# Performance work log

Hardware: AMD Instinct MI355X
Metric: run time of the kernel (lower is better)

Reference implementation:

```python
import jax, jax.numpy as jnp
import numpy as np

HEAD_DIM = 64
NORM_EPS = 1e-5
W_SCALE = -0.6065306597126334  # -exp(-0.5)


def _rwkv7_scan(r, w, k, v, a, b):
    # r,w,k,a,b: [B,T,H,K]; v: [B,T,H,V]. Official RWKV7 recurrence (per head):
    #   S_t = S_{t-1} * diag(exp(w_t)) + (S_{t-1} @ a_t) b_t^T + v_t k_t^T ,  o_t = S_t @ r_t
    Bsz, T, H, K = r.shape
    V = v.shape[-1]
    decay = jnp.exp(w)

    def step(S, xs):
        r_t, d_t, k_t, v_t, a_t, b_t = xs
        sa = jnp.einsum('bhvk,bhk->bhv', S, a_t)
        S = S * d_t[:, :, None, :] + sa[..., None] * b_t[:, :, None, :] + v_t[..., None] * k_t[:, :, None, :]
        o_t = jnp.einsum('bhvk,bhk->bhv', S, r_t)
        return S, o_t

    xs = tuple(jnp.moveaxis(t, 1, 0) for t in (r, decay, k, v, a, b))
    S0 = jnp.zeros((Bsz, H, V, K), dtype=r.dtype)
    _, o = jax.lax.scan(step, S0, xs)
    return jnp.moveaxis(o, 0, 1)  # [B,T,H,V]


def setup_inputs() -> dict:
    key = jax.random.key(0)
    B, T, H = 2, 4096, 2048
    NH, DK, DV = 32, 64, 64
    D_DECAY, D_A, D_V, D_G = 96, 96, 64, 256
    ks = iter(jax.random.split(key, 40))
    n = lambda *s: jax.random.normal(next(ks), s, dtype=jnp.float32)
    u = lambda *s: jax.random.uniform(next(ks), s, dtype=jnp.float32)
    inp = {
        'hidden_states': n(B, T, H),
        'v_first': n(B, T, H),
        'x_r': u(1, 1, H), 'x_w': u(1, 1, H), 'x_k': u(1, 1, H),
        'x_v': u(1, 1, H), 'x_a': u(1, 1, H), 'x_g': u(1, 1, H),
        'k_k': 0.71 + 0.05 * n(H),
        'k_a': 1.02 + 0.05 * n(H),
        'r_k': -0.04 + 0.02 * n(NH, DK),
        'w_r': 0.02 * n(H, H), 'w_k': 0.002 * n(H, H),
        'w_v': 0.02 * n(H, H), 'w_o': 0.02 * n(H, H),
        'wA': 0.02 * n(D_DECAY, H), 'wB': 0.02 * n(H, D_DECAY), 'wb': -0.5 + 0.1 * n(H),
        'aA': 0.02 * n(D_A, H), 'aB': 0.02 * n(H, D_A), 'ab': 0.1 * n(H),
        'vA': 0.02 * n(D_V, H), 'vB': 0.02 * n(H, D_V), 'vb': 0.5 + 0.1 * n(H),
        'gA': 0.02 * n(D_G, H), 'gB': 0.02 * n(H, D_G),
        'gn_w': jnp.ones(H, jnp.float32),
        'gn_b': jnp.zeros(H, jnp.float32),
    }
    return inp


def reference(hidden_states, v_first, x_r, x_w, x_k, x_v, x_a, x_g,
              k_k, k_a, r_k, w_r, w_k, w_v, w_o,
              wA, wB, wb, aA, aB, ab, vA, vB, vb, gA, gB, gn_w, gn_b):
    B, T, H = hidden_states.shape
    NH, DK = r_k.shape
    DV = H // NH
    # token shift: delta = shift(x) - x (zero-padded at t=0)
    shifted = jnp.pad(hidden_states, ((0, 0), (1, 0), (0, 0)))[:, :-1]
    delta = shifted - hidden_states
    xr = hidden_states + delta * x_r
    xw = hidden_states + delta * x_w
    xk = hidden_states + delta * x_k
    xv = hidden_states + delta * x_v
    xa = hidden_states + delta * x_a
    xg = hidden_states + delta * x_g
    r = xr @ w_r.T
    w = W_SCALE * jax.nn.sigmoid(jnp.tanh(xw @ wA.T) @ wB.T + wb)  # log-decay in (-0.6065, 0)
    k = xk @ w_k.T
    v = xv @ w_v.T
    v = v + (v_first - v) * jax.nn.sigmoid((xv @ vA.T) @ vB.T + vb)  # lerp with v_first (layer_idx != 0)
    a = jax.nn.sigmoid((xa @ aA.T) @ aB.T + ab)
    g = jax.nn.sigmoid(xg @ gA.T) @ gB.T  # g_lora: sigmoid activation inside, no bias
    kk = (k * k_k).reshape(B, T, NH, DK)
    kk = kk / jnp.maximum(jnp.linalg.norm(kk, axis=-1, keepdims=True), 1e-12)
    k = k * (1.0 + (a - 1.0) * k_a)  # fused_k_rwkv7
    r4 = r.reshape(B, T, NH, DK)
    w4 = w.reshape(B, T, NH, DK)
    k4 = k.reshape(B, T, NH, DK)
    a4 = a.reshape(B, T, NH, DK)
    v4 = v.reshape(B, T, NH, DV)
    o = _rwkv7_scan(r4, w4, k4, v4, -kk, kk * a4)  # [B,T,NH,DV]
    # GroupNorm over each head (eps = head_dim * norm_eps)
    mu = o.mean(-1, keepdims=True)
    var = ((o - mu) ** 2).mean(-1, keepdims=True)
    on = (o - mu) / jnp.sqrt(var + HEAD_DIM * NORM_EPS)
    on = on * gn_w.reshape(NH, DV) + gn_b.reshape(NH, DV)
    on = on + (r4 * k4 * r_k).sum(-1, keepdims=True) * v4
    out = (on.reshape(B, T, H) * g) @ w_o.T
    return out
```

## Files before the change

kernel.cpp:

```cpp
#include <hip/hip_runtime.h>
#include <cstdint>
#include <cstddef>

typedef unsigned short u16;
typedef unsigned int u32;

typedef __bf16 bf8_t __attribute__((ext_vector_type(8)));
typedef float f4_t __attribute__((ext_vector_type(4)));

__device__ __forceinline__ u16 f2bf(float x) {
  u32 u = __float_as_uint(x);
  u = (u + 0x7fffu + ((u >> 16) & 1u)) >> 16;
  return (u16)u;
}
__device__ __forceinline__ float bf2f(u16 x) {
  u32 u = ((u32)x) << 16;
  return __uint_as_float(u);
}
__device__ __forceinline__ float sigf(float x) { return 1.f / (1.f + __expf(-x)); }

#define MFMA16(a, b, c) __builtin_amdgcn_mfma_f32_16x16x32_bf16(a, b, c, 0, 0, 0)

__global__ void fill_kernel(float* p, float v, long n) {
  long i = (long)blockIdx.x * blockDim.x + threadIdx.x;
  if (i < n) p[i] = v;
}

__global__ void padcvt_kernel(const float* __restrict__ src, u16* __restrict__ dst,
                              int rows, int cols, int pc, long total) {
  long i = (long)blockIdx.x * blockDim.x + threadIdx.x;
  if (i >= total) return;
  int r = (int)(i / pc), c = (int)(i % pc);
  float v = (r < rows && c < cols) ? src[(long)r * cols + c] : 0.f;
  dst[i] = f2bf(v);
}

__global__ void wf_kernel(const float* __restrict__ src, const float* __restrict__ coef,
                          u16* __restrict__ Wf, int rows_valid, int row0, long total) {
  long i = (long)blockIdx.x * blockDim.x + threadIdx.x;
  if (i >= total) return;
  int r = (int)(i >> 12);
  int k = (int)(i & 4095);
  float v = 0.f;
  if (r < rows_valid) {
    int kk = k & 2047;
    v = src[(long)r * 2048 + kk];
    if (k >= 2048) v *= coef[kk];
  }
  Wf[(long)(row0 + r) * 4096 + k] = f2bf(v);
}

__global__ void hd_kernel(const float* __restrict__ h_b, u16* __restrict__ out_seg,
                          int t0, int Tc, long total4) {
  long i = (long)blockIdx.x * blockDim.x + threadIdx.x;
  if (i >= total4) return;
  long e = i * 4;
  const int H = 2048;
  int col = (int)(e % H);
  int tl = (int)(e / H);
  int tg = t0 + tl;
  const float* hp = h_b + (long)tg * H + col;
  float4 hv = *(const float4*)hp;
  float4 pv = make_float4(0.f, 0.f, 0.f, 0.f);
  if (tg > 0) pv = *(const float4*)(hp - H);
  u16* row = out_seg + (long)tl * 4096;
  uint2 ph, pd;
  ph.x = (u32)f2bf(hv.x) | ((u32)f2bf(hv.y) << 16);
  ph.y = (u32)f2bf(hv.z) | ((u32)f2bf(hv.w) << 16);
  pd.x = (u32)f2bf(pv.x - hv.x) | ((u32)f2bf(pv.y - hv.y) << 16);
  pd.y = (u32)f2bf(pv.z - hv.z) | ((u32)f2bf(pv.w - hv.w) << 16);
  *(uint2*)(row + col) = ph;
  *(uint2*)(row + 2048 + col) = pd;
}

__global__ void mix1_kernel(const float* __restrict__ h_b, const float* __restrict__ coef,
                            u16* __restrict__ out_seg, int t0, int Tc, long total4) {
  long i = (long)blockIdx.x * blockDim.x + threadIdx.x;
  if (i >= total4) return;
  long e = i * 4;
  const int H = 2048;
  int col = (int)(e % H);
  int tl = (int)(e / H);
  int tg = t0 + tl;
  const float* hp = h_b + (long)tg * H + col;
  float4 hv = *(const float4*)hp;
  float4 pv = make_float4(0.f, 0.f, 0.f, 0.f);
  if (tg > 0) pv = *(const float4*)(hp - H);
  float4 cc = *(const float4*)(coef + col);
  uint2 pk;
  pk.x = (u32)f2bf(hv.x + (pv.x - hv.x) * cc.x) | ((u32)f2bf(hv.y + (pv.y - hv.y) * cc.y) << 16);
  pk.y = (u32)f2bf(hv.z + (pv.z - hv.z) * cc.z) | ((u32)f2bf(hv.w + (pv.w - hv.w) * cc.w) << 16);
  *(uint2*)(out_seg + e) = pk;
}

#define LDSW 40
template <int MODE>
__global__ __launch_bounds__(256) void gemm_bt(
    const u16* __restrict__ A, const u16* __restrict__ B, void* __restrict__ Cv,
    int M, int N, int K, int lda, const float* __restrict__ aux1) {
  __shared__ u16 sA[128 * LDSW];
  __shared__ u16 sB[128 * LDSW];
  const int tid = threadIdx.x;
  const long bm = (long)blockIdx.y * 128;
  const long bn = (long)blockIdx.x * 128;
  const int wave = tid >> 6, lane = tid & 63;
  const int wm = (wave >> 1) * 64, wn = (wave & 1) * 64;
  const int quad = lane >> 4, rr = lane & 15;

  f4_t acc[4][4];
  const f4_t zero = {0.f, 0.f, 0.f, 0.f};
#pragma unroll
  for (int i = 0; i < 4; i++)
#pragma unroll
    for (int j = 0; j < 4; j++) acc[i][j] = zero;

  const int c0 = tid, c1 = tid + 256;
  const u16* pa0 = A + (bm + (c0 >> 2)) * (long)lda + (c0 & 3) * 8;
  const u16* pa1 = A + (bm + (c1 >> 2)) * (long)lda + (c1 & 3) * 8;
  const u16* pb0 = B + (bn + (c0 >> 2)) * (long)K + (c0 & 3) * 8;
  const u16* pb1 = B + (bn + (c1 >> 2)) * (long)K + (c1 & 3) * 8;

  uint4 ra0, ra1, rb0, rb1;
#define LDG(k0)                              \
  {                                          \
    ra0 = *(const uint4*)(pa0 + (k0));       \
    ra1 = *(const uint4*)(pa1 + (k0));       \
    rb0 = *(const uint4*)(pb0 + (k0));       \
    rb1 = *(const uint4*)(pb1 + (k0));       \
  }
  LDG(0);
  for (int k0 = 0; k0 < K; k0 += 32) {
    __syncthreads();
    *(uint4*)(&sA[(c0 >> 2) * LDSW + (c0 & 3) * 8]) = ra0;
    *(uint4*)(&sA[(c1 >> 2) * LDSW + (c1 & 3) * 8]) = ra1;
    *(uint4*)(&sB[(c0 >> 2) * LDSW + (c0 & 3) * 8]) = rb0;
    *(uint4*)(&sB[(c1 >> 2) * LDSW + (c1 & 3) * 8]) = rb1;
    __syncthreads();
    if (k0 + 32 < K) LDG(k0 + 32);
    bf8_t af[4], bfv[4];
#pragma unroll
    for (int i = 0; i < 4; i++)
      af[i] = *(const bf8_t*)(&sA[(wm + i * 16 + rr) * LDSW + quad * 8]);
#pragma unroll
    for (int j = 0; j < 4; j++)
      bfv[j] = *(const bf8_t*)(&sB[(wn + j * 16 + rr) * LDSW + quad * 8]);
#pragma unroll
    for (int i = 0; i < 4; i++)
#pragma unroll
      for (int j = 0; j < 4; j++)
        acc[i][j] = MFMA16(af[i], bfv[j], acc[i][j]);
  }
#undef LDG
#pragma unroll
  for (int i = 0; i < 4; i++)
#pragma unroll
    for (int j = 0; j < 4; j++)
#pragma unroll
      for (int rg = 0; rg < 4; rg++) {
        long m = bm + wm + i * 16 + quad * 4 + rg;
        long n = bn + wn + j * 16 + rr;
        long id = m * (long)N + n;
        float x = acc[i][j][rg];
        if (MODE == 0) ((float*)Cv)[id] = x;
        else if (MODE == 1) ((u16*)Cv)[id] = f2bf(x);
        else if (MODE == 2) ((u16*)Cv)[id] = f2bf(tanhf(x));
        else if (MODE == 3) ((u16*)Cv)[id] = f2bf(sigf(x));
        else if (MODE == 5) {
          float y = (n < 128) ? tanhf(x) : ((n < 384) ? x : sigf(x));
          ((u16*)Cv)[id] = f2bf(y);
        } else if (MODE == 6) {
          ((u16*)Cv)[id] = f2bf(sigf(x + aux1[(int)n]));
        }
      }
}

__device__ __forceinline__ void gload16(const u16* g, u16* l) {
  __builtin_amdgcn_global_load_lds((const __attribute__((address_space(1))) u32*)g,
                                   (__attribute__((address_space(3))) u32*)l, 16, 0, 0);
}

template <int MODE>
__global__ __launch_bounds__(512, 2) void gemm256_bt(
    const u16* __restrict__ A, const u16* __restrict__ Bw, void* __restrict__ Cv,
    int M, int N, int K, int rsp, long r0off, long r1off) {
  __shared__ u16 L[2][2][2][8192];
  const int tid = threadIdx.x;
  const int lane = tid & 63, w = tid >> 6;
  const int quad = lane >> 4, l15 = lane & 15;
  const long bm = (long)blockIdx.y * 256, bn = (long)blockIdx.x * 256;
  const int wm = (w >> 2) * 128, wn = (w & 3) * 64;
  const int NT = K >> 6;

  const int u0 = tid, u1 = tid + 512;
  const int ar0 = u0 >> 2, ar1 = u1 >> 2;
  const int aq0 = (u0 & 3) ^ (ar0 & 3), aq1 = (u1 & 3) ^ (ar1 & 3);
  const u16* gA0 = A + (bm + ar0) * (long)K + aq0 * 8;
  const u16* gA1 = A + (bm + ar1) * (long)K + aq1 * 8;
  const u16* gB0 = Bw + (bn + ar0) * (long)K + aq0 * 8;
  const u16* gB1 = Bw + (bn + ar1) * (long)K + aq1 * 8;

  const int qx = (quad ^ (l15 & 3)) * 8;
  const int roA = (wm + l15) * 32 + qx;
  const int roB = (wn + l15) * 32 + qx;

  f4_t acc[8][4];
#pragma unroll
  for (int i = 0; i < 8; i++)
#pragma unroll
    for (int j = 0; j < 4; j++) acc[i][j] = (f4_t){0.f, 0.f, 0.f, 0.f};

#define STG_A(buf, s, tt)                                   \
  {                                                         \
    long ko = ((long)(tt) << 6) + ((s) << 5);               \
    gload16(gA0 + ko, &L[buf][0][s][u0 * 8]);               \
    gload16(gA1 + ko, &L[buf][0][s][u1 * 8]);               \
  }
#define STG_B(buf, s, tt)                                   \
  {                                                         \
    long ko = ((long)(tt) << 6) + ((s) << 5);               \
    gload16(gB0 + ko, &L[buf][1][s][u0 * 8]);               \
    gload16(gB1 + ko, &L[buf][1][s][u1 * 8]);               \
  }
#define LDA4(P, o)                                          \
  _Pragma("unroll") for (int i = 0; i < 4; i++)             \
      aF[i] = *(const bf8_t*)((P) + roA + ((o) + i) * 512);
#define LDB4(P)                                             \
  _Pragma("unroll") for (int j = 0; j < 4; j++)             \
      bF[j] = *(const bf8_t*)((P) + roB + j * 512);
#define MFMA_BLK(base)                                      \
  __builtin_amdgcn_s_setprio(1);                            \
  _Pragma("unroll") for (int i = 0; i < 4; i++)             \
      _Pragma("unroll") for (int j = 0; j < 4; j++)         \
          acc[(base) + i][j] = MFMA16(aF[i], bF[j], acc[(base) + i][j]); \
  __builtin_amdgcn_s_setprio(0);
#define SBAR __builtin_amdgcn_s_barrier()

  STG_A(0, 0, 0); STG_B(0, 0, 0);
  STG_A(0, 1, 0); STG_B(0, 1, 0);
  if (NT > 1) { STG_A(1, 0, 1); STG_B(1, 0, 1); }
  asm volatile("s_waitcnt vmcnt(8)" ::: "memory");
  SBAR;

  bf8_t aF[4], bF[4];
  for (int t = 0; t < NT; ++t) {
    const int buf = t & 1;
    const u16* A0 = &L[buf][0][0][0];
    const u16* B0 = &L[buf][1][0][0];
    const u16* A1 = &L[buf][0][1][0];
    const u16* B1 = &L[buf][1][1][0];
    LDA4(A0, 0);
    LDB4(B0);
    if (t + 1 < NT) STG_A(buf ^ 1, 1, t + 1);
    SBAR;
    asm volatile("s_waitcnt lgkmcnt(0)" ::: "memory");
    MFMA_BLK(0);
    SBAR;
    LDA4(A0, 4);
    if (t + 1 < NT) STG_B(buf ^ 1, 1, t + 1);
    SBAR;
    asm volatile("s_waitcnt lgkmcnt(0)" ::: "memory");
    MFMA_BLK(4);
    if (t == NT - 1) asm volatile("s_waitcnt vmcnt(0)" ::: "memory");
    else asm volatile("s_waitcnt vmcnt(8)" ::: "memory");
    SBAR;
    LDA4(A1, 0);
    LDB4(B1);
    if (t + 2 < NT) STG_A(buf, 0, t + 2);
    SBAR;
    asm volatile("s_waitcnt lgkmcnt(0)" ::: "memory");
    MFMA_BLK(0);
    SBAR;
    LDA4(A1, 4);
    if (t + 2 < NT) STG_B(buf, 0, t + 2);
    SBAR;
    asm volatile("s_waitcnt lgkmcnt(0)" ::: "memory");
    MFMA_BLK(4);
    if (t == NT - 2) asm volatile("s_waitcnt vmcnt(4)" ::: "memory");
    else if (t < NT - 2) asm volatile("s_waitcnt vmcnt(8)" ::: "memory");
    SBAR;
  }

#pragma unroll
  for (int i = 0; i < 8; i++) {
#pragma unroll
    for (int rg = 0; rg < 4; rg++) {
      long mm = bm + wm + i * 16 + quad * 4 + rg;
      long crow = (mm < rsp) ? (mm + r0off) : (mm + r1off);
#pragma unroll
      for (int j = 0; j < 4; j++) {
        long n = bn + wn + j * 16 + l15;
        float x = acc[i][j][rg];
        if (MODE == 0) ((float*)Cv)[crow * (long)N + n] = x;
        else ((u16*)Cv)[crow * (long)N + n] = f2bf(x);
      }
    }
  }
#undef STG_A
#undef STG_B
#undef LDA4
#undef LDB4
#undef MFMA_BLK
#undef SBAR
}

__global__ __launch_bounds__(256) void post1_kernel(
    const float* __restrict__ F1, const float* __restrict__ F4, float* F0,
    const float* __restrict__ F2, const u16* __restrict__ VL,
    const float* __restrict__ vfirst,
    u16* __restrict__ KM, u16* __restrict__ KK, u16* __restrict__ BB, u16* __restrict__ VB,
    const float* __restrict__ k_k, const float* __restrict__ k_a,
    const float* __restrict__ wb, const float* __restrict__ ab, int t0, int Tc) {
  const int lane = threadIdx.x & 63;
  const long th = (((long)blockIdx.x * 256) + threadIdx.x) >> 6;
  const int hcol = (int)(th & 31) * 64 + lane;
  const long idx = th * 64 + lane;
  const long r = th >> 5;
  float kraw = F1[idx];
  float kk0 = kraw * k_k[hcol];
  float ss = kk0 * kk0;
#pragma unroll
  for (int m = 32; m; m >>= 1) ss += __shfl_xor(ss, m, 64);
  float kkn = kk0 / fmaxf(sqrtf(ss), 1e-12f);
  float av = sigf(F4[idx] + ab[hcol]);
  float w = -0.6065306597126334f * sigf(F0[idx] + wb[hcol]);
  F0[idx] = w;
  KM[idx] = f2bf(kraw * (1.f + (av - 1.f) * k_a[hcol]));
  KK[idx] = f2bf(kkn);
  BB[idx] = f2bf(kkn * av);
  float vraw = F2[idx];
  float sg = bf2f(VL[idx]);
  long vfi = ((r / Tc) * 4096 + t0 + (r % Tc)) * 2048 + hcol;
  VB[idx] = f2bf(vraw + (vfirst[vfi] - vraw) * sg);
}

constexpr int ST64 = 72;
constexpr int ST32 = 40;
constexpr int STX = 132;

__global__ __launch_bounds__(64) void phaseA_kernel(
    const float* __restrict__ wS, const u16* __restrict__ kmS, const u16* __restrict__ kkS,
    const u16* __restrict__ bbS, const u16* __restrict__ vbS, const u16* __restrict__ rbS,
    float* __restrict__ POWb, u16* __restrict__ PAb, float* __restrict__ Zb,
    u16* __restrict__ GTb, float* __restrict__ CLb, int Tc, int sp0) {
  __shared__ u16 lXa[16 * ST64], lXr[16 * ST64], lYa[16 * ST64], lYb[16 * ST64];
  __shared__ u16 lYaT[64 * ST32], lYbT[64 * ST32], lVmT[64 * ST32];
  __shared__ u16 lTWt[64 * ST32], lTAt[64 * ST32];
  __shared__ u16 lP[16 * ST32], lQ[16 * ST32], lBm[16 * ST32];
  __shared__ float lA[16 * 16];
  __shared__ float lX[16 * STX];
  __shared__ float lcl[64];
  const int lane = threadIdx.x;
  const int quad = lane >> 4, l15 = lane & 15;
  const long tile = blockIdx.x;
  const int bh = (int)(tile & 63);
  const int col = (int)(tile >> 6);
  const int b = bh >> 5, h = bh & 31;
  const long s = tile;
  const f4_t z4 = {0.f, 0.f, 0.f, 0.f};

  {
    u32* p0 = (u32*)&lYaT[lane * ST32 + 16];
    u32* p1 = (u32*)&lYbT[lane * ST32 + 16];
    u32* p2 = (u32*)&lVmT[lane * ST32 + 16];
    u32* p3 = (u32*)&lTWt[lane * ST32 + 16];
    u32* p4 = (u32*)&lTAt[lane * ST32 + 16];
#pragma unroll
    for (int q = 0; q < 8; q++) { p0[q] = 0; p1[q] = 0; p2[q] = 0; p3[q] = 0; p4[q] = 0; }
    if (lane < 16) {
      u32* q0 = (u32*)&lP[lane * ST32 + 16];
      u32* q1 = (u32*)&lQ[lane * ST32 + 16];
      u32* q2 = (u32*)&lBm[lane * ST32 + 16];
#pragma unroll
      for (int q = 0; q < 8; q++) { q0[q] = 0; q1[q] = 0; q2[q] = 0; }
    }
  }

  const long rowbase = (long)b * Tc + (long)(sp0 + col) * 16;
  const long gbase = rowbase * 2048 + (long)h * 64 + lane;
  float cw = 0.f;
#pragma unroll
  for (int i = 0; i < 16; i++) {
    long g = gbase + (long)i * 2048;
    float w = wS[g];
    float km = bf2f(kmS[g]), kk = bf2f(kkS[g]), bb = bf2f(bbS[g]);
    float vv = bf2f(vbS[g]), rr2 = bf2f(rbS[g]);
    float cwm = cw;
    cw += w;
    float E1 = __expf(cwm), E2 = __expf(-cw), E3 = __expf(cw);
    float xa = -kk * E1;
    lXa[i * ST64 + lane] = f2bf(xa);
    lX[i * STX + 64 + lane] = xa;
    lXr[i * ST64 + lane] = f2bf(rr2 * E3);
    float ya = bb * E2, yb = km * E2;
    lYa[i * ST64 + lane] = f2bf(ya);
    lYb[i * ST64 + lane] = f2bf(yb);
    lYaT[lane * ST32 + i] = f2bf(ya);
    lYbT[lane * ST32 + i] = f2bf(yb);
    lVmT[lane * ST32 + i] = f2bf(vv);
    if (i == 15) { lcl[lane] = E3; CLb[s * 64 + lane] = E3; }
  }
  __syncthreads();

  {
    f4_t aA = z4, aB = z4, aP = z4, aQ = z4;
#pragma unroll
    for (int kc = 0; kc < 2; kc++) {
      bf8_t xa = *(const bf8_t*)&lXa[l15 * ST64 + quad * 8 + 32 * kc];
      bf8_t xr = *(const bf8_t*)&lXr[l15 * ST64 + quad * 8 + 32 * kc];
      bf8_t ya = *(const bf8_t*)&lYa[l15 * ST64 + quad * 8 + 32 * kc];
      bf8_t yb = *(const bf8_t*)&lYb[l15 * ST64 + quad * 8 + 32 * kc];
      aA = MFMA16(xa, ya, aA);
      aB = MFMA16(xa, yb, aB);
      aP = MFMA16(xr, ya, aP);
      aQ = MFMA16(xr, yb, aQ);
    }
#pragma unroll
    for (int rg = 0; rg < 4; rg++) {
      int m = quad * 4 + rg;
      lA[m * 16 + l15] = (l15 < m) ? aA[rg] : 0.f;
      lBm[m * ST32 + l15] = (l15 < m) ? f2bf(aB[rg]) : (u16)0;
      lP[m * ST32 + l15] = (l15 <= m) ? f2bf(aP[rg]) : (u16)0;
      lQ[m * ST32 + l15] = (l15 <= m) ? f2bf(aQ[rg]) : (u16)0;
    }
  }
  __syncthreads();

#pragma unroll
  for (int nt = 0; nt < 4; nt++) {
    f4_t acc = z4;
    bf8_t a = *(const bf8_t*)&lBm[l15 * ST32 + quad * 8];
    bf8_t bb2 = *(const bf8_t*)&lVmT[(nt * 16 + l15) * ST32 + quad * 8];
    acc = MFMA16(a, bb2, acc);
#pragma unroll
    for (int rg = 0; rg < 4; rg++) lX[(quad * 4 + rg) * STX + nt * 16 + l15] = acc[rg];
  }
  __syncthreads();

  for (int i = 1; i < 16; i++) {
    float x0 = lX[i * STX + lane], x1 = lX[i * STX + 64 + lane];
    for (int j = 0; j < i; j++) {
      float aij = lA[i * 16 + j];
      x0 += aij * lX[j * STX + lane];
      x1 += aij * lX[j * STX + 64 + lane];
    }
    lX[i * STX + lane] = x0;
    lX[i * STX + 64 + lane] = x1;
  }
#pragma unroll
  for (int i = 0; i < 16; i++) {
    lTWt[lane * ST32 + i] = f2bf(lX[i * STX + lane]);
    lTAt[lane * ST32 + i] = f2bf(lX[i * STX + 64 + lane]);
  }
  __syncthreads();

#pragma unroll
  for (int nt = 0; nt < 4; nt++) {
    f4_t acc = z4;
    bf8_t p = *(const bf8_t*)&lP[l15 * ST32 + quad * 8];
    bf8_t q = *(const bf8_t*)&lQ[l15 * ST32 + quad * 8];
    bf8_t tw = *(const bf8_t*)&lTWt[(nt * 16 + l15) * ST32 + quad * 8];
    bf8_t vm = *(const bf8_t*)&lVmT[(nt * 16 + l15) * ST32 + quad * 8];
    acc = MFMA16(p, tw, acc);
    acc = MFMA16(q, vm, acc);
#pragma unroll
    for (int rg = 0; rg < 4; rg++)
      POWb[s * 1024 + (quad * 4 + rg) * 64 + nt * 16 + l15] = acc[rg];
  }
#pragma unroll
  for (int nt = 0; nt < 4; nt++) {
    f4_t acc = z4;
    bf8_t p = *(const bf8_t*)&lP[l15 * ST32 + quad * 8];
    bf8_t ta = *(const bf8_t*)&lTAt[(nt * 16 + l15) * ST32 + quad * 8];
    acc = MFMA16(p, ta, acc);
#pragma unroll
    for (int rg = 0; rg < 4; rg++) {
      float xr = bf2f(lXr[(quad * 4 + rg) * ST64 + nt * 16 + l15]);
      PAb[s * 1024 + (quad * 4 + rg) * 64 + nt * 16 + l15] = f2bf(acc[rg] + xr);
    }
  }

#pragma unroll
  for (int mt = 0; mt < 4; mt++)
#pragma unroll
    for (int nt = 0; nt < 4; nt++) {
      f4_t acc = z4;
      bf8_t tw = *(const bf8_t*)&lTWt[(mt * 16 + l15) * ST32 + quad * 8];
      bf8_t vm = *(const bf8_t*)&lVmT[(mt * 16 + l15) * ST32 + quad * 8];
      bf8_t yat = *(const bf8_t*)&lYaT[(nt * 16 + l15) * ST32 + quad * 8];
      bf8_t ybt = *(const bf8_t*)&lYbT[(nt * 16 + l15) * ST32 + quad * 8];
      acc = MFMA16(tw, yat, acc);
      acc = MFMA16(vm, ybt, acc);
      float cl = lcl[nt * 16 + l15];
#pragma unroll
      for (int rg = 0; rg < 4; rg++)
        Zb[s * 4096 + (mt * 16 + quad * 4 + rg) * 64 + nt * 16 + l15] = acc[rg] * cl;
    }
#pragma unroll
  for (int mt = 0; mt < 4; mt++)
#pragma unroll
    for (int nt = 0; nt < 4; nt++) {
      f4_t acc = z4;
      bf8_t yat = *(const bf8_t*)&lYaT[(mt * 16 + l15) * ST32 + quad * 8];
      bf8_t ta = *(const bf8_t*)&lTAt[(nt * 16 + l15) * ST32 + quad * 8];
      acc = MFMA16(yat, ta, acc);
#pragma unroll
      for (int rg = 0; rg < 4; rg++) {
        float cl = lcl[mt * 16 + quad * 4 + rg];
        GTb[s * 4096 + (mt * 16 + quad * 4 + rg) * 64 + nt * 16 + l15] = f2bf(acc[rg] * cl);
      }
    }
}

__global__ __launch_bounds__(256) void phaseB_kernel(
    const float* __restrict__ Zb, const u16* __restrict__ GTb, const float* __restrict__ CLb,
    u16* __restrict__ S0b, float* __restrict__ state, int CT, int init) {
  __shared__ u16 Sb[64 * ST64];
  const int bh = blockIdx.x;
  const int tid = threadIdx.x, wv = tid >> 6, lane = tid & 63;
  const int quad = lane >> 4, l15 = lane & 15;
  float S[4][4];
  if (init) {
#pragma unroll
    for (int nt = 0; nt < 4; nt++)
#pragma unroll
      for (int rg = 0; rg < 4; rg++) S[nt][rg] = 0.f;
  } else {
#pragma unroll
    for (int nt = 0; nt < 4; nt++)
#pragma unroll
      for (int rg = 0; rg < 4; rg++)
        S[nt][rg] = state[(long)bh * 4096 + (16 * wv + quad * 4 + rg) * 64 + nt * 16 + l15];
  }
  const f4_t z4 = {0.f, 0.f, 0.f, 0.f};
  for (int c = 0; c < CT; c++) {
    long s = (long)c * 64 + bh;
#pragma unroll
    for (int nt = 0; nt < 4; nt++)
#pragma unroll
      for (int rg = 0; rg < 4; rg++)
        Sb[(16 * wv + quad * 4 + rg) * ST64 + nt * 16 + l15] = f2bf(S[nt][rg]);
    __syncthreads();
    f4_t acc[4] = {z4, z4, z4, z4};
#pragma unroll
    for (int kc = 0; kc < 2; kc++) {
      bf8_t a = *(const bf8_t*)&Sb[(16 * wv + l15) * ST64 + quad * 8 + 32 * kc];
      *(uint4*)(S0b + s * 4096 + (16 * wv + l15) * 64 + quad * 8 + 32 * kc) = *(uint4*)&a;
#pragma unroll
      for (int nt = 0; nt < 4; nt++) {
        bf8_t g = *(const bf8_t*)(GTb + s * 4096 + (nt * 16 + l15) * 64 + quad * 8 + 32 * kc);
        acc[nt] = MFMA16(a, g, acc[nt]);
      }
    }
#pragma unroll
    for (int nt = 0; nt < 4; nt++) {
      float cl = CLb[s * 64 + nt * 16 + l15];
#pragma unroll
      for (int rg = 0; rg < 4; rg++) {
        float z = Zb[s * 4096 + (16 * wv + quad * 4 + rg) * 64 + nt * 16 + l15];
        S[nt][rg] = S[nt][rg] * cl + acc[nt][rg] + z;
      }
    }
    __syncthreads();
  }
#pragma unroll
  for (int nt = 0; nt < 4; nt++)
#pragma unroll
    for (int rg = 0; rg < 4; rg++)
      state[(long)bh * 4096 + (16 * wv + quad * 4 + rg) * 64 + nt * 16 + l15] = S[nt][rg];
}

__global__ __launch_bounds__(64) void phaseC_kernel(
    const float* __restrict__ POWb, const u16* __restrict__ PAb, const u16* __restrict__ S0b,
    float* __restrict__ O, int Tc, int sp0) {
  const int lane = threadIdx.x, quad = lane >> 4, l15 = lane & 15;
  const long tile = blockIdx.x;
  const int bh = (int)(tile & 63), col = (int)(tile >> 6);
  const int b = bh >> 5, h = bh & 31;
  const long s = tile;
  const f4_t z4 = {0.f, 0.f, 0.f, 0.f};
  f4_t acc[4] = {z4, z4, z4, z4};
#pragma unroll
  for (int kc = 0; kc < 2; kc++) {
    bf8_t a = *(const bf8_t*)(PAb + s * 1024 + l15 * 64 + quad * 8 + 32 * kc);
#pragma unroll
    for (int nt = 0; nt < 4; nt++) {
      bf8_t bo = *(const bf8_t*)(S0b + s * 4096 + (nt * 16 + l15) * 64 + quad * 8 + 32 * kc);
      acc[nt] = MFMA16(a, bo, acc[nt]);
    }
  }
  const long rowbase = (long)b * Tc + (long)(sp0 + col) * 16;
#pragma unroll
  for (int nt = 0; nt < 4; nt++)
#pragma unroll
    for (int rg = 0; rg < 4; rg++) {
      int i = quad * 4 + rg, v = nt * 16 + l15;
      float p = POWb[s * 1024 + i * 64 + v];
      O[(rowbase + i) * 2048 + (long)h * 64 + v] = p + acc[nt][rg];
    }
}

__global__ __launch_bounds__(256) void epi_kernel(
    const float* __restrict__ o, const u16* __restrict__ r, const u16* __restrict__ k,
    const u16* __restrict__ v, const u16* __restrict__ g,
    const float* __restrict__ r_k, const float* __restrict__ gn_w, const float* __restrict__ gn_b,
    u16* __restrict__ y) {
  const int lane = threadIdx.x & 63;
  const long th = (((long)blockIdx.x * 256) + threadIdx.x) >> 6;
  const int hcol = (int)(th & 31) * 64 + lane;
  const long idx = th * 64 + lane;
  float ov = o[idx];
  float s = ov;
#pragma unroll
  for (int m = 32; m; m >>= 1) s += __shfl_xor(s, m, 64);
  float mu = s * (1.f / 64.f);
  float d = ov - mu;
  float vs = d * d;
#pragma unroll
  for (int m = 32; m; m >>= 1) vs += __shfl_xor(vs, m, 64);
  float on = d * rsqrtf(vs * (1.f / 64.f) + 6.4e-4f);
  on = on * gn_w[hcol] + gn_b[hcol];
  float rk = bf2f(r[idx]) * bf2f(k[idx]) * r_k[hcol];
#pragma unroll
  for (int m = 32; m; m >>= 1) rk += __shfl_xor(rk, m, 64);
  on += rk * bf2f(v[idx]);
  y[idx] = f2bf(on * bf2f(g[idx]));
}

extern "C" void kernel_launch(void* const* d_in, const int* in_sizes, int n_in,
                              void* d_out, int out_size, void* d_ws, size_t ws_size,
                              hipStream_t stream) {
  constexpr int B = 2, T = 4096, H = 2048;
  const float* hst    = (const float*)d_in[0];
  const float* vfirst = (const float*)d_in[1];
  const float* x_r = (const float*)d_in[2];
  const float* x_w = (const float*)d_in[3];
  const float* x_k = (const float*)d_in[4];
  const float* x_v = (const float*)d_in[5];
  const float* x_a = (const float*)d_in[6];
  const float* x_g = (const float*)d_in[7];
  const float* k_k = (const float*)d_in[8];
  const float* k_a = (const float*)d_in[9];
  const float* r_k = (const float*)d_in[10];
  const float* w_r = (const float*)d_in[11];
  const float* w_k = (const float*)d_in[12];
  const float* w_v = (const float*)d_in[13];
  const float* w_o = (const float*)d_in[14];
  const float* wA  = (const float*)d_in[15];
  const float* wB  = (const float*)d_in[16];
  const float* wb  = (const float*)d_in[17];
  const float* aA  = (const float*)d_in[18];
  const float* aB  = (const float*)d_in[19];
  const float* ab  = (const float*)d_in[20];
  const float* vA  = (const float*)d_in[21];
  const float* vB  = (const float*)d_in[22];
  const float* vb  = (const float*)d_in[23];
  const float* gA  = (const float*)d_in[24];
  const float* gB  = (const float*)d_in[25];
  const float* gn_w= (const float*)d_in[26];
  const float* gn_b= (const float*)d_in[27];

  const size_t WEIGHT_BYTES = 4 * (size_t)H * H * 2 + 3 * (size_t)H * 128 * 2
                            + (size_t)H * 256 * 2 + (size_t)768 * 4096 * 2;
  const size_t STATE_BYTES = (size_t)64 * 4096 * 4;
  const size_t TILE_BYTES = 4096 + 2048 + 16384 + 8192 + 256 + 8192;

  int NC = -1, CT = 0;
  for (int pass = 0; pass < 2 && NC < 0; pass++) {
    for (int nc : {1, 2, 4, 8, 16}) {
      long Tc_ = T / nc;
      long R_ = (long)B * Tc_;
      long RH_ = R_ * H;
      size_t base = (size_t)RH_ * 16 + (size_t)RH_ * 16 + (size_t)RH_ * 4 + (size_t)R_ * 1536
                  + WEIGHT_BYTES + STATE_BYTES + (4 << 20);
      int cols = (int)(Tc_ / 16);
      int found = 0;
      for (int ct : {64, 32, 16, 8}) {
        if (ct > cols) continue;
        if (pass == 0 && ct < 16) continue;
        size_t need = base + (size_t)64 * ct * TILE_BYTES;
        if (need <= ws_size) { NC = nc; CT = ct; found = 1; break; }
      }
      if (found) break;
    }
  }
  const int BS = 256;
  auto cdiv = [](long a, long b) { return (int)((a + b - 1) / b); };
  if (NC < 0) {
    fill_kernel<<<cdiv(out_size, BS), BS, 0, stream>>>(
        (float*)d_out, 200000.f + (float)(ws_size >> 20), out_size);
    return;
  }
  const int Tc = T / NC;
  const long R = (long)B * Tc;
  const long RH = R * H;
  const int cols = Tc / 16;
  const int NTILE = 64 * CT;

  char* ws = (char*)d_ws;
  size_t off = 0;
  auto alloc = [&](size_t bytes) -> void* {
    void* p = ws + off;
    off += (bytes + 255) & ~(size_t)255;
    return p;
  };
  float* F0 = (float*)alloc(RH * 4);
  float* F1 = (float*)alloc(RH * 4);
  float* F2 = (float*)alloc(RH * 4);
  float* F4 = (float*)alloc(RH * 4);
  u16* KM  = (u16*)alloc(RH * 2);
  u16* KK  = (u16*)alloc(RH * 2);
  u16* BBs = (u16*)alloc(RH * 2);
  u16* VBs = (u16*)alloc(RH * 2);
  u16* RBs = (u16*)alloc(RH * 2);
  u16* MIXB = (u16*)alloc(RH * 2);
  u16* G    = (u16*)alloc(RH * 2);
  u16* VL   = (u16*)alloc(RH * 2);
  u16* HD   = (u16*)alloc(RH * 4);
  u16* s1all = (u16*)alloc(R * 1536);
  u16* wrb = (u16*)alloc((size_t)H * H * 2);
  u16* wkb = (u16*)alloc((size_t)H * H * 2);
  u16* wvb = (u16*)alloc((size_t)H * H * 2);
  u16* wob = (u16*)alloc((size_t)H * H * 2);
  u16* wBb = (u16*)alloc((size_t)H * 128 * 2);
  u16* aBb = (u16*)alloc((size_t)H * 128 * 2);
  u16* vBb = (u16*)alloc((size_t)H * 128 * 2);
  u16* gBb = (u16*)alloc((size_t)H * 256 * 2);
  u16* Wf  = (u16*)alloc((size_t)768 * 4096 * 2);
  float* state = (float*)alloc(STATE_BYTES);
  float* POWb = (float*)alloc((size_t)NTILE * 4096);
  u16*   PAb  = (u16*)alloc((size_t)NTILE * 2048);
  float* Zb   = (float*)alloc((size_t)NTILE * 16384);
  u16*   GTb  = (u16*)alloc((size_t)NTILE * 8192);
  float* CLb  = (float*)alloc((size_t)NTILE * 256);
  u16*   S0b  = (u16*)alloc((size_t)NTILE * 8192);
  float* Ob = F1;

  padcvt_kernel<<<cdiv((long)H * H, BS), BS, 0, stream>>>(w_r, wrb, H, H, H, (long)H * H);
  padcvt_kernel<<<cdiv((long)H * H, BS), BS, 0, stream>>>(w_k, wkb, H, H, H, (long)H * H);
  padcvt_kernel<<<cdiv((long)H * H, BS), BS, 0, stream>>>(w_v, wvb, H, H, H, (long)H * H);
  padcvt_kernel<<<cdiv((long)H * H, BS), BS, 0, stream>>>(w_o, wob, H, H, H, (long)H * H);
  padcvt_kernel<<<cdiv((long)H * 128, BS), BS, 0, stream>>>(wB, wBb, H, 96, 128, (long)H * 128);
  padcvt_kernel<<<cdiv((long)H * 128, BS), BS, 0, stream>>>(aB, aBb, H, 96, 128, (long)H * 128);
  padcvt_kernel<<<cdiv((long)H * 128, BS), BS, 0, stream>>>(vB, vBb, H, 64, 128, (long)H * 128);
  padcvt_kernel<<<cdiv((long)H * 256, BS), BS, 0, stream>>>(gB, gBb, H, 256, 256, (long)H * 256);
  wf_kernel<<<cdiv((long)128 * 4096, BS), BS, 0, stream>>>(wA, x_w, Wf, 96, 0, (long)128 * 4096);
  wf_kernel<<<cdiv((long)128 * 4096, BS), BS, 0, stream>>>(aA, x_a, Wf, 96, 128, (long)128 * 4096);
  wf_kernel<<<cdiv((long)128 * 4096, BS), BS, 0, stream>>>(vA, x_v, Wf, 64, 256, (long)128 * 4096);
  wf_kernel<<<cdiv((long)384 * 4096, BS), BS, 0, stream>>>(gA, x_g, Wf, 256, 384, (long)384 * 4096);

  const long mixTot = (long)Tc * H / 4;
  const int mixG = cdiv(mixTot, BS);
  const int ehG = (int)(R * 32 / 4);

  for (int c = 0; c < NC; c++) {
    const int t0 = c * Tc;
    auto MIX = [&](const float* coef) {
      for (int b = 0; b < B; b++)
        mix1_kernel<<<mixG, BS, 0, stream>>>(hst + (long)b * T * H, coef,
                                             MIXB + (long)b * Tc * H, t0, Tc, mixTot);
    };
    dim3 gBig(16, (unsigned)(R / 128)), gF(6, (unsigned)(R / 128));
    dim3 g256((unsigned)(H / 256), (unsigned)(R / 256));

    for (int b = 0; b < B; b++)
      hd_kernel<<<mixG, BS, 0, stream>>>(hst + (long)b * T * H,
                                         HD + (long)b * Tc * 4096, t0, Tc, mixTot);
    gemm_bt<5><<<gF, 256, 0, stream>>>(HD, Wf, s1all, (int)R, 768, 4096, 4096, nullptr);
    gemm_bt<0><<<gBig, 256, 0, stream>>>(s1all, wBb, F0, (int)R, H, 128, 768, nullptr);
    gemm_bt<0><<<gBig, 256, 0, stream>>>(s1all + 128, aBb, F4, (int)R, H, 128, 768, nullptr);
    MIX(x_v);
    gemm256_bt<0><<<g256, 512, 0, stream>>>(MIXB, wvb, F2, (int)R, H, H, (int)R, 0, 0);
    gemm_bt<6><<<gBig, 256, 0, stream>>>(s1all + 256, vBb, VL, (int)R, H, 128, 768, vb);
    gemm_bt<1><<<gBig, 256, 0, stream>>>(s1all + 384, gBb, G, (int)R, H, 256, 768, nullptr);
    MIX(x_r);
    gemm256_bt<1><<<g256, 512, 0, stream>>>(MIXB, wrb, RBs, (int)R, H, H, (int)R, 0, 0);
    MIX(x_k);
    gemm256_bt<0><<<g256, 512, 0, stream>>>(MIXB, wkb, F1, (int)R, H, H, (int)R, 0, 0);
    post1_kernel<<<ehG, 256, 0, stream>>>(F1, F4, F0, F2, VL, vfirst,
                                          KM, KK, BBs, VBs, k_k, k_a, wb, ab, t0, Tc);
    for (int sp = 0; sp < cols; sp += CT) {
      phaseA_kernel<<<NTILE, 64, 0, stream>>>(F0, KM, KK, BBs, VBs, RBs,
                                              POWb, PAb, Zb, GTb, CLb, Tc, sp);
      phaseB_kernel<<<64, 256, 0, stream>>>(Zb, GTb, CLb, S0b, state, CT,
                                            (c == 0 && sp == 0) ? 1 : 0);
      phaseC_kernel<<<NTILE, 64, 0, stream>>>(POWb, PAb, S0b, Ob, Tc, sp);
    }
    epi_kernel<<<ehG, 256, 0, stream>>>(Ob, RBs, KM, VBs, G, r_k, gn_w, gn_b, MIXB);
    gemm256_bt<0><<<g256, 512, 0, stream>>>(MIXB, wob, (float*)d_out, (int)R, H, H,
                                            Tc, (long)t0, (long)T - Tc + t0);
  }
}
```

Before: 2.852 ms.

## Prefetch phaseB chunk inputs, double-buffer gemm_bt loads, merge decay/a LoRA GEMMs

```diff
diff --git a/kernel.cpp b/kernel.cpp
--- a/kernel.cpp
+++ b/kernel.cpp
@@ -48,6 +48,17 @@
     if (k >= 2048) v *= coef[kk];
   }
   Wf[(long)(row0 + r) * 4096 + k] = f2bf(v);
+}
+
+__global__ void wab_kernel(const float* __restrict__ wB, const float* __restrict__ aB,
+                           u16* __restrict__ Wab, long total) {
+  long i = (long)blockIdx.x * blockDim.x + threadIdx.x;
+  if (i >= total) return;
+  int r = (int)(i >> 8), k = (int)(i & 255);
+  float v = 0.f;
+  if (r < 2048) { if (k < 96) v = wB[(long)r * 96 + k]; }
+  else { int rr = r - 2048; if (k >= 128 && k < 224) v = aB[(long)rr * 96 + (k - 128)]; }
+  Wab[i] = f2bf(v);
 }
 
 __global__ void hd_kernel(const float* __restrict__ h_b, u16* __restrict__ out_seg,
@@ -120,37 +131,58 @@
   const u16* pb0 = B + (bn + (c0 >> 2)) * (long)K + (c0 & 3) * 8;
   const u16* pb1 = B + (bn + (c1 >> 2)) * (long)K + (c1 & 3) * 8;
 
-  uint4 ra0, ra1, rb0, rb1;
-#define LDG(k0)                              \
-  {                                          \
-    ra0 = *(const uint4*)(pa0 + (k0));       \
-    ra1 = *(const uint4*)(pa1 + (k0));       \
-    rb0 = *(const uint4*)(pb0 + (k0));       \
-    rb1 = *(const uint4*)(pb1 + (k0));       \
-  }
-  LDG(0);
-  for (int k0 = 0; k0 < K; k0 += 32) {
+  uint4 a0A, a1A, b0A, b1A, a0B, a1B, b0B, b1B;
+#define LDGA(k0)                            \
+  {                                         \
+    a0A = *(const uint4*)(pa0 + (k0));      \
+    a1A = *(const uint4*)(pa1 + (k0));      \
+    b0A = *(const uint4*)(pb0 + (k0));      \
+    b1A = *(const uint4*)(pb1 + (k0));      \
+  }
+#define LDGB(k0)                            \
+  {                                         \
+    a0B = *(const uint4*)(pa0 + (k0));      \
+    a1B = *(const uint4*)(pa1 + (k0));      \
+    b0B = *(const uint4*)(pb0 + (k0));      \
+    b1B = *(const uint4*)(pb1 + (k0));      \
+  }
+#define STLDS(ra0, ra1, rb0, rb1)                          \
+  {                                                        \
+    *(uint4*)(&sA[(c0 >> 2) * LDSW + (c0 & 3) * 8]) = ra0; \
+    *(uint4*)(&sA[(c1 >> 2) * LDSW + (c1 & 3) * 8]) = ra1; \
+    *(uint4*)(&sB[(c0 >> 2) * LDSW + (c0 & 3) * 8]) = rb0; \
+    *(uint4*)(&sB[(c1 >> 2) * LDSW + (c1 & 3) * 8]) = rb1; \
+  }
+#define COMPUTE                                                        \
+  {                                                                    \
+    bf8_t af[4], bfv[4];                                               \
+    _Pragma("unroll") for (int i = 0; i < 4; i++)                      \
+        af[i] = *(const bf8_t*)(&sA[(wm + i * 16 + rr) * LDSW + quad * 8]); \
+    _Pragma("unroll") for (int j = 0; j < 4; j++)                      \
+        bfv[j] = *(const bf8_t*)(&sB[(wn + j * 16 + rr) * LDSW + quad * 8]); \
+    _Pragma("unroll") for (int i = 0; i < 4; i++)                      \
+        _Pragma("unroll") for (int j = 0; j < 4; j++)                  \
+            acc[i][j] = MFMA16(af[i], bfv[j], acc[i][j]);              \
+  }
+
+  LDGA(0);
+  LDGB(32);
+  for (int k0 = 0; k0 < K; k0 += 64) {
     __syncthreads();
-    *(uint4*)(&sA[(c0 >> 2) * LDSW + (c0 & 3) * 8]) = ra0;
-    *(uint4*)(&sA[(c1 >> 2) * LDSW + (c1 & 3) * 8]) = ra1;
-    *(uint4*)(&sB[(c0 >> 2) * LDSW + (c0 & 3) * 8]) = rb0;
-    *(uint4*)(&sB[(c1 >> 2) * LDSW + (c1 & 3) * 8]) = rb1;
+    STLDS(a0A, a1A, b0A, b1A);
     __syncthreads();
-    if (k0 + 32 < K) LDG(k0 + 32);
-    bf8_t af[4], bfv[4];
-#pragma unroll
-    for (int i = 0; i < 4; i++)
-      af[i] = *(const bf8_t*)(&sA[(wm + i * 16 + rr) * LDSW + quad * 8]);
-#pragma unroll
-    for (int j = 0; j < 4; j++)
-      bfv[j] = *(const bf8_t*)(&sB[(wn + j * 16 + rr) * LDSW + quad * 8]);
-#pragma unroll
-    for (int i = 0; i < 4; i++)
-#pragma unroll
-      for (int j = 0; j < 4; j++)
-        acc[i][j] = MFMA16(af[i], bfv[j], acc[i][j]);
-  }
-#undef LDG
+    if (k0 + 64 < K) LDGA(k0 + 64);
+    COMPUTE;
+    __syncthreads();
+    STLDS(a0B, a1B, b0B, b1B);
+    __syncthreads();
+    if (k0 + 96 < K) LDGB(k0 + 96);
+    COMPUTE;
+  }
+#undef LDGA
+#undef LDGB
+#undef STLDS
+#undef COMPUTE
 #pragma unroll
   for (int i = 0; i < 4; i++)
 #pragma unroll
@@ -304,7 +336,7 @@
 }
 
 __global__ __launch_bounds__(256) void post1_kernel(
-    const float* __restrict__ F1, const float* __restrict__ F4, float* F0,
+    const float* __restrict__ F1, const float* __restrict__ F0F4, float* __restrict__ W,
     const float* __restrict__ F2, const u16* __restrict__ VL,
     const float* __restrict__ vfirst,
     u16* __restrict__ KM, u16* __restrict__ KK, u16* __restrict__ BB, u16* __restrict__ VB,
@@ -321,9 +353,11 @@
 #pragma unroll
   for (int m = 32; m; m >>= 1) ss += __shfl_xor(ss, m, 64);
   float kkn = kk0 / fmaxf(sqrtf(ss), 1e-12f);
-  float av = sigf(F4[idx] + ab[hcol]);
-  float w = -0.6065306597126334f * sigf(F0[idx] + wb[hcol]);
-  F0[idx] = w;
+  float wlog = F0F4[r * 4096 + hcol];
+  float alog = F0F4[r * 4096 + 2048 + hcol];
+  float av = sigf(alog + ab[hcol]);
+  float w = -0.6065306597126334f * sigf(wlog + wb[hcol]);
+  W[idx] = w;
   KM[idx] = f2bf(kraw * (1.f + (av - 1.f) * k_a[hcol]));
   KK[idx] = f2bf(kkn);
   BB[idx] = f2bf(kkn * av);
@@ -532,36 +566,52 @@
         S[nt][rg] = state[(long)bh * 4096 + (16 * wv + quad * 4 + rg) * 64 + nt * 16 + l15];
   }
   const f4_t z4 = {0.f, 0.f, 0.f, 0.f};
-  for (int c = 0; c < CT; c++) {
-    long s = (long)c * 64 + bh;
-#pragma unroll
-    for (int nt = 0; nt < 4; nt++)
-#pragma unroll
-      for (int rg = 0; rg < 4; rg++)
-        Sb[(16 * wv + quad * 4 + rg) * ST64 + nt * 16 + l15] = f2bf(S[nt][rg]);
-    __syncthreads();
-    f4_t acc[4] = {z4, z4, z4, z4};
-#pragma unroll
-    for (int kc = 0; kc < 2; kc++) {
-      bf8_t a = *(const bf8_t*)&Sb[(16 * wv + l15) * ST64 + quad * 8 + 32 * kc];
-      *(uint4*)(S0b + s * 4096 + (16 * wv + l15) * 64 + quad * 8 + 32 * kc) = *(uint4*)&a;
-#pragma unroll
-      for (int nt = 0; nt < 4; nt++) {
-        bf8_t g = *(const bf8_t*)(GTb + s * 4096 + (nt * 16 + l15) * 64 + quad * 8 + 32 * kc);
-        acc[nt] = MFMA16(a, g, acc[nt]);
-      }
-    }
-#pragma unroll
-    for (int nt = 0; nt < 4; nt++) {
-      float cl = CLb[s * 64 + nt * 16 + l15];
-#pragma unroll
-      for (int rg = 0; rg < 4; rg++) {
-        float z = Zb[s * 4096 + (16 * wv + quad * 4 + rg) * 64 + nt * 16 + l15];
-        S[nt][rg] = S[nt][rg] * cl + acc[nt][rg] + z;
-      }
-    }
-    __syncthreads();
-  }
+
+  uint4 gtA[2][4], gtB[2][4];
+  float zA[4][4], zB[4][4], clA[4], clB[4];
+
+#define LOADSET(cc, gt, z, cl)                                                      \
+  {                                                                                 \
+    long s2 = (long)(cc) * 64 + bh;                                                 \
+    _Pragma("unroll") for (int kc = 0; kc < 2; kc++)                                \
+        _Pragma("unroll") for (int nt = 0; nt < 4; nt++)                            \
+            gt[kc][nt] = *(const uint4*)(GTb + s2 * 4096 + (nt * 16 + l15) * 64 + quad * 8 + 32 * kc); \
+    _Pragma("unroll") for (int nt = 0; nt < 4; nt++) {                              \
+      cl[nt] = CLb[s2 * 64 + nt * 16 + l15];                                        \
+      _Pragma("unroll") for (int rg = 0; rg < 4; rg++)                              \
+          z[nt][rg] = Zb[s2 * 4096 + (16 * wv + quad * 4 + rg) * 64 + nt * 16 + l15]; \
+    }                                                                               \
+  }
+#define BSTEP(cc, gt, z, cl, gtN, zN, clN, pf)                                      \
+  {                                                                                 \
+    long s1 = (long)(cc) * 64 + bh;                                                 \
+    _Pragma("unroll") for (int nt = 0; nt < 4; nt++)                                \
+        _Pragma("unroll") for (int rg = 0; rg < 4; rg++)                            \
+            Sb[(16 * wv + quad * 4 + rg) * ST64 + nt * 16 + l15] = f2bf(S[nt][rg]); \
+    __syncthreads();                                                                \
+    if (pf) LOADSET((cc) + 1, gtN, zN, clN);                                        \
+    f4_t acc[4] = {z4, z4, z4, z4};                                                 \
+    _Pragma("unroll") for (int kc = 0; kc < 2; kc++) {                              \
+      bf8_t a = *(const bf8_t*)&Sb[(16 * wv + l15) * ST64 + quad * 8 + 32 * kc];    \
+      *(uint4*)(S0b + s1 * 4096 + (16 * wv + l15) * 64 + quad * 8 + 32 * kc) = *(uint4*)&a; \
+      _Pragma("unroll") for (int nt = 0; nt < 4; nt++) {                            \
+        bf8_t g = *(const bf8_t*)&gt[kc][nt];                                       \
+        acc[nt] = MFMA16(a, g, acc[nt]);                                            \
+      }                                                                             \
+    }                                                                               \
+    _Pragma("unroll") for (int nt = 0; nt < 4; nt++)                                \
+        _Pragma("unroll") for (int rg = 0; rg < 4; rg++)                            \
+            S[nt][rg] = S[nt][rg] * cl[nt] + acc[nt][rg] + z[nt][rg];               \
+    __syncthreads();                                                                \
+  }
+
+  LOADSET(0, gtA, zA, clA);
+  for (int c = 0; c < CT; c += 2) {
+    BSTEP(c, gtA, zA, clA, gtB, zB, clB, (c + 1 < CT));
+    BSTEP(c + 1, gtB, zB, clB, gtA, zA, clA, (c + 2 < CT));
+  }
+#undef LOADSET
+#undef BSTEP
 #pragma unroll
   for (int nt = 0; nt < 4; nt++)
 #pragma unroll
@@ -659,8 +709,9 @@
   const float* gn_w= (const float*)d_in[26];
   const float* gn_b= (const float*)d_in[27];
 
-  const size_t WEIGHT_BYTES = 4 * (size_t)H * H * 2 + 3 * (size_t)H * 128 * 2
-                            + (size_t)H * 256 * 2 + (size_t)768 * 4096 * 2;
+  const size_t WEIGHT_BYTES = 4 * (size_t)H * H * 2 + (size_t)H * 128 * 2
+                            + (size_t)H * 256 * 2 + (size_t)768 * 4096 * 2
+                            + (size_t)4096 * 256 * 2;
   const size_t STATE_BYTES = (size_t)64 * 4096 * 4;
   const size_t TILE_BYTES = 4096 + 2048 + 16384 + 8192 + 256 + 8192;
 
@@ -670,7 +721,7 @@
       long Tc_ = T / nc;
       long R_ = (long)B * Tc_;
       long RH_ = R_ * H;
-      size_t base = (size_t)RH_ * 16 + (size_t)RH_ * 16 + (size_t)RH_ * 4 + (size_t)R_ * 1536
+      size_t base = (size_t)RH_ * 40 + (size_t)R_ * 1536
                   + WEIGHT_BYTES + STATE_BYTES + (4 << 20);
       int cols = (int)(Tc_ / 16);
       int found = 0;
@@ -703,10 +754,10 @@
     off += (bytes + 255) & ~(size_t)255;
     return p;
   };
-  float* F0 = (float*)alloc(RH * 4);
+  float* F0F4 = (float*)alloc(RH * 8);
   float* F1 = (float*)alloc(RH * 4);
   float* F2 = (float*)alloc(RH * 4);
-  float* F4 = (float*)alloc(RH * 4);
+  float* W  = (float*)alloc(RH * 4);
   u16* KM  = (u16*)alloc(RH * 2);
   u16* KK  = (u16*)alloc(RH * 2);
   u16* BBs = (u16*)alloc(RH * 2);
@@ -721,11 +772,10 @@
   u16* wkb = (u16*)alloc((size_t)H * H * 2);
   u16* wvb = (u16*)alloc((size_t)H * H * 2);
   u16* wob = (u16*)alloc((size_t)H * H * 2);
-  u16* wBb = (u16*)alloc((size_t)H * 128 * 2);
-  u16* aBb = (u16*)alloc((size_t)H * 128 * 2);
   u16* vBb = (u16*)alloc((size_t)H * 128 * 2);
   u16* gBb = (u16*)alloc((size_t)H * 256 * 2);
   u16* Wf  = (u16*)alloc((size_t)768 * 4096 * 2);
+  u16* Wab = (u16*)alloc((size_t)4096 * 256 * 2);
   float* state = (float*)alloc(STATE_BYTES);
   float* POWb = (float*)alloc((size_t)NTILE * 4096);
   u16*   PAb  = (u16*)alloc((size_t)NTILE * 2048);
@@ -739,14 +789,13 @@
   padcvt_kernel<<<cdiv((long)H * H, BS), BS, 0, stream>>>(w_k, wkb, H, H, H, (long)H * H);
   padcvt_kernel<<<cdiv((long)H * H, BS), BS, 0, stream>>>(w_v, wvb, H, H, H, (long)H * H);
   padcvt_kernel<<<cdiv((long)H * H, BS), BS, 0, stream>>>(w_o, wob, H, H, H, (long)H * H);
-  padcvt_kernel<<<cdiv((long)H * 128, BS), BS, 0, stream>>>(wB, wBb, H, 96, 128, (long)H * 128);
-  padcvt_kernel<<<cdiv((long)H * 128, BS), BS, 0, stream>>>(aB, aBb, H, 96, 128, (long)H * 128);
   padcvt_kernel<<<cdiv((long)H * 128, BS), BS, 0, stream>>>(vB, vBb, H, 64, 128, (long)H * 128);
   padcvt_kernel<<<cdiv((long)H * 256, BS), BS, 0, stream>>>(gB, gBb, H, 256, 256, (long)H * 256);
   wf_kernel<<<cdiv((long)128 * 4096, BS), BS, 0, stream>>>(wA, x_w, Wf, 96, 0, (long)128 * 4096);
   wf_kernel<<<cdiv((long)128 * 4096, BS), BS, 0, stream>>>(aA, x_a, Wf, 96, 128, (long)128 * 4096);
   wf_kernel<<<cdiv((long)128 * 4096, BS), BS, 0, stream>>>(vA, x_v, Wf, 64, 256, (long)128 * 4096);
   wf_kernel<<<cdiv((long)384 * 4096, BS), BS, 0, stream>>>(gA, x_g, Wf, 256, 384, (long)384 * 4096);
+  wab_kernel<<<cdiv((long)4096 * 256, BS), BS, 0, stream>>>(wB, aB, Wab, (long)4096 * 256);
 
   const long mixTot = (long)Tc * H / 4;
   const int mixG = cdiv(mixTot, BS);
@@ -759,15 +808,14 @@
         mix1_kernel<<<mixG, BS, 0, stream>>>(hst + (long)b * T * H, coef,
                                              MIXB + (long)b * Tc * H, t0, Tc, mixTot);
     };
-    dim3 gBig(16, (unsigned)(R / 128)), gF(6, (unsigned)(R / 128));
+    dim3 gBig(16, (unsigned)(R / 128)), gF(6, (unsigned)(R / 128)), gWA(32, (unsigned)(R / 128));
     dim3 g256((unsigned)(H / 256), (unsigned)(R / 256));
 
     for (int b = 0; b < B; b++)
       hd_kernel<<<mixG, BS, 0, stream>>>(hst + (long)b * T * H,
                                          HD + (long)b * Tc * 4096, t0, Tc, mixTot);
     gemm_bt<5><<<gF, 256, 0, stream>>>(HD, Wf, s1all, (int)R, 768, 4096, 4096, nullptr);
-    gemm_bt<0><<<gBig, 256, 0, stream>>>(s1all, wBb, F0, (int)R, H, 128, 768, nullptr);
-    gemm_bt<0><<<gBig, 256, 0, stream>>>(s1all + 128, aBb, F4, (int)R, H, 128, 768, nullptr);
+    gemm_bt<0><<<gWA, 256, 0, stream>>>(s1all, Wab, F0F4, (int)R, 4096, 256, 768, nullptr);
     MIX(x_v);
     gemm256_bt<0><<<g256, 512, 0, stream>>>(MIXB, wvb, F2, (int)R, H, H, (int)R, 0, 0);
     gemm_bt<6><<<gBig, 256, 0, stream>>>(s1all + 256, vBb, VL, (int)R, H, 128, 768, vb);
@@ -776,10 +824,10 @@
     gemm256_bt<1><<<g256, 512, 0, stream>>>(MIXB, wrb, RBs, (int)R, H, H, (int)R, 0, 0);
     MIX(x_k);
     gemm256_bt<0><<<g256, 512, 0, stream>>>(MIXB, wkb, F1, (int)R, H, H, (int)R, 0, 0);
-    post1_kernel<<<ehG, 256, 0, stream>>>(F1, F4, F0, F2, VL, vfirst,
+    post1_kernel<<<ehG, 256, 0, stream>>>(F1, F0F4, W, F2, VL, vfirst,
                                           KM, KK, BBs, VBs, k_k, k_a, wb, ab, t0, Tc);
     for (int sp = 0; sp < cols; sp += CT) {
-      phaseA_kernel<<<NTILE, 64, 0, stream>>>(F0, KM, KK, BBs, VBs, RBs,
+      phaseA_kernel<<<NTILE, 64, 0, stream>>>(W, KM, KK, BBs, VBs, RBs,
                                               POWb, PAb, Zb, GTb, CLb, Tc, sp);
       phaseB_kernel<<<64, 256, 0, stream>>>(Zb, GTb, CLb, S0b, state, CT,
                                             (c == 0 && sp == 0) ? 1 : 0);
```

New measurement: 2.745 ms. -3.8%, faster.
